# Performance work log

Hardware: AMD Instinct MI355X
Metric: run time of the kernel (lower is better)

The kernel has to match this reference:

```python
import jax, jax.numpy as jnp
import numpy as np

B, S, D, U = 32, 2048, 512, 512

def setup_inputs() -> dict:
    key = jax.random.key(0)
    k1, k2, k3, k4, k5 = jax.random.split(key, 5)
    passage = jax.random.normal(k1, (B, S, D), dtype=jnp.float32)
    hidden = jax.random.normal(k2, (B, D), dtype=jnp.float32)
    mask = jnp.ones((B, S), dtype=jnp.float32)
    # learned params (Dense kernels, glorot-ish scale)
    W1 = jax.random.normal(k3, (D, U), dtype=jnp.float32) / np.sqrt(D)
    W2 = jax.random.normal(k4, (D, U), dtype=jnp.float32) / np.sqrt(D)
    Vw = jax.random.normal(k5, (U, 1), dtype=jnp.float32) / np.sqrt(U)
    Vb = jnp.zeros((1,), dtype=jnp.float32)
    return {"passage": passage, "hidden": hidden, "mask": mask,
            "W1": W1, "W2": W2, "Vw": Vw, "Vb": Vb}

def reference(passage, hidden, mask, W1, W2, Vw, Vb):
    # passage: [B,S,D], hidden: [B,D], mask: [B,S]
    h_proj = jnp.einsum('bd,du->bu', hidden, W2)[:, None, :]        # [B,1,U]
    p_proj = jnp.einsum('bsd,du->bsu', passage, W1)                  # [B,S,U]
    score = jnp.einsum('bsu,uo->bso', jnp.tanh(p_proj + h_proj), Vw) + Vb  # [B,S,1]
    score = score + ((1.0 - mask) * -1e30)[:, :, None]
    attention_weights = jax.nn.softmax(score, axis=1)                # [B,S,1]
    context_vector = jnp.sum(attention_weights * passage, axis=1)    # [B,D]
    return context_vector, attention_weights
```

## Files before the change

kernel.cpp:

```cpp
#include <hip/hip_runtime.h>
#include <hip/hip_bf16.h>
#include <cstddef>


#define NB 32
#define NS 2048
#define ND 512
#define NU 512

typedef __bf16 bf16_t;
typedef __bf16 bf16x8 __attribute__((ext_vector_type(8)));
typedef float floatx4 __attribute__((ext_vector_type(4)));

__device__ __forceinline__ void dma16(const void* g, void* l) {
    __builtin_amdgcn_global_load_lds(
        (const __attribute__((address_space(1))) unsigned int*)g,
        (__attribute__((address_space(3))) unsigned int*)l, 16, 0, 0);
}

__global__ __launch_bounds__(256) void prep_kernel(
    const float* __restrict__ W1, bf16_t* __restrict__ W1p,
    const float* __restrict__ hidden, const float* __restrict__ W2,
    float* __restrict__ hproj) {
    if (blockIdx.x < 128) {
        int wave = threadIdx.x >> 6, lane = threadIdx.x & 63;
        int f = (blockIdx.x << 2) + wave;
        int kc = f >> 5, ng = f & 31;
        int q = lane >> 4, c = lane & 15;
        const float* src = W1 + (kc * 32 + q * 8) * 512 + ng * 16 + c;
        bf16x8 w;
#pragma unroll
        for (int jj = 0; jj < 8; ++jj) w[jj] = (bf16_t)src[jj * 512];
        ((bf16x8*)W1p)[(f << 6) + lane] = w;
    } else {
        __shared__ float h[ND];
        __shared__ float part[256];
        int bi = blockIdx.x - 128;
        int b = bi >> 2, ug = bi & 3;
        int t = threadIdx.x;
        h[t] = hidden[b * ND + t];
        h[t + 256] = hidden[b * ND + t + 256];
        __syncthreads();
        int u = (ug << 7) + (t & 127);
        int d0 = (t >> 7) << 8;
        float acc = 0.f;
#pragma unroll 8
        for (int d = d0; d < d0 + 256; ++d) acc = fmaf(h[d], W2[d * NU + u], acc);
        part[t] = acc;
        __syncthreads();
        if (t < 128) hproj[b * NU + u] = part[t] + part[t + 128];
    }
}

__global__ __launch_bounds__(256, 3) void score_kernel(
    const float* __restrict__ passage, const bf16_t* __restrict__ W1p,
    const float* __restrict__ hproj, const float* __restrict__ Vw,
    const float* __restrict__ Vb, float* __restrict__ scores) {
    __shared__ float ring[4 * 64 * 32];
    __shared__ float red[4 * 64];
    const int tid = threadIdx.x;
    const int wave = tid >> 6, lane = tid & 63;
    const int q = lane >> 4, c = lane & 15;
    const int bid = blockIdx.x;
    const int mblk = ((bid >> 4) << 3) + (bid & 7);
    const int nhalf = (bid >> 3) & 1;
    const int m0 = mblk * 64;
    const int b = m0 >> 11;
    const int ng0 = (nhalf << 4) + (wave << 2);
    const bf16x8* Wq = (const bf16x8*)W1p;

    const int ch0 = wave * 2;
    const int r0 = ch0 * 8 + (lane >> 3);
    const int k0 = ((lane & 7) - r0) & 7;
    const int r1 = r0 + 8;
    const int k1 = ((lane & 7) - r1) & 7;
    const float* g0 = passage + (size_t)(m0 + r0) * ND + k0 * 4;
    const float* g1 = passage + (size_t)(m0 + r1) * ND + k1 * 4;

#define DMA_SLICE(slice) do {                                         \
        char* _l = (char*)ring + ((slice) & 3) * 8192 + ch0 * 1024;   \
        dma16(g0 + (slice) * 32, _l);                                 \
        dma16(g1 + (slice) * 32, _l + 1024);                          \
    } while (0)

    DMA_SLICE(0);
    DMA_SLICE(1);
    DMA_SLICE(2);
    asm volatile("" ::: "memory");
    bf16x8 bb[2][4];
#pragma unroll
    for (int j = 0; j < 4; ++j)
        bb[0][j] = Wq[((ng0 + j) << 6) + lane];
    asm volatile("s_waitcnt vmcnt(8)" ::: "memory");
    __builtin_amdgcn_s_barrier();

    floatx4 acc[4][4];
#pragma unroll
    for (int i = 0; i < 4; ++i)
#pragma unroll
        for (int j = 0; j < 4; ++j) { floatx4 z = {0.f, 0.f, 0.f, 0.f}; acc[i][j] = z; }

#pragma unroll
    for (int kc = 0; kc < 16; ++kc) {
        if (kc < 15) {
#pragma unroll
            for (int j = 0; j < 4; ++j)
                bb[(kc + 1) & 1][j] = Wq[((((kc + 1) << 5) + ng0 + j) << 6) + lane];
        }
        if (kc + 3 < 16) DMA_SLICE(kc + 3);

        const float* sl = ring + (kc & 3) * 2048;
#pragma unroll
        for (int i = 0; i < 4; ++i) {
            int r = i * 16 + c;
            const float* rp = sl + r * 32;
            floatx4 lo = *(const floatx4*)(rp + (((q << 1) + r) & 7) * 4);
            floatx4 hi = *(const floatx4*)(rp + (((q << 1) + 1 + r) & 7) * 4);
            bf16x8 a;
            a[0] = (bf16_t)lo[0]; a[1] = (bf16_t)lo[1];
            a[2] = (bf16_t)lo[2]; a[3] = (bf16_t)lo[3];
            a[4] = (bf16_t)hi[0]; a[5] = (bf16_t)hi[1];
            a[6] = (bf16_t)hi[2]; a[7] = (bf16_t)hi[3];
#pragma unroll
            for (int j = 0; j < 4; ++j)
                acc[i][j] = __builtin_amdgcn_mfma_f32_16x16x32_bf16(a, bb[kc & 1][j], acc[i][j], 0, 0, 0);
        }
        if (kc < 15) {
            asm volatile("s_waitcnt vmcnt(8)" ::: "memory");
            __builtin_amdgcn_s_barrier();
        }
    }
#undef DMA_SLICE

    float sp[4][4];
#pragma unroll
    for (int i = 0; i < 4; ++i)
#pragma unroll
        for (int r = 0; r < 4; ++r) sp[i][r] = 0.f;
#pragma unroll
    for (int j = 0; j < 4; ++j) {
        int n = ((ng0 + j) << 4) + c;
        float hp = hproj[(b << 9) + n];
        float vw = Vw[n];
#pragma unroll
        for (int i = 0; i < 4; ++i)
#pragma unroll
            for (int r = 0; r < 4; ++r) {
                float x = acc[i][j][r] + hp;
                float e = __expf(2.0f * x);
                float t = 1.0f - 2.0f * __builtin_amdgcn_rcpf(e + 1.0f);
                sp[i][r] = fmaf(t, vw, sp[i][r]);
            }
    }
#pragma unroll
    for (int off = 1; off < 16; off <<= 1)
#pragma unroll
        for (int i = 0; i < 4; ++i)
#pragma unroll
            for (int r = 0; r < 4; ++r)
                sp[i][r] += __shfl_xor(sp[i][r], off, 64);

    if (c == 0) {
#pragma unroll
        for (int i = 0; i < 4; ++i)
#pragma unroll
            for (int r = 0; r < 4; ++r)
                red[(wave << 6) + i * 16 + q * 4 + r] = sp[i][r];
    }
    __syncthreads();
    if (tid < 64) {
        float s = red[tid] + red[64 + tid] + red[128 + tid] + red[192 + tid];
        if (nhalf == 0) s += Vb[0];
        atomicAdd(&scores[m0 + tid], s);
    }
}

__global__ __launch_bounds__(1024) void softmax_kernel(
    const float* __restrict__ mask, float* __restrict__ attn) {
    __shared__ float smx[16], ssm[16];
    int b = blockIdx.x, tid = threadIdx.x;
    int wave = tid >> 6, lane = tid & 63;
    const int base = b * NS;
    float v0 = attn[base + tid] + (1.0f - mask[base + tid]) * (-1e30f);
    float v1 = attn[base + 1024 + tid] + (1.0f - mask[base + 1024 + tid]) * (-1e30f);
    float mx = fmaxf(v0, v1);
#pragma unroll
    for (int off = 1; off < 64; off <<= 1) mx = fmaxf(mx, __shfl_xor(mx, off, 64));
    if (lane == 0) smx[wave] = mx;
    __syncthreads();
    mx = smx[0];
#pragma unroll
    for (int w = 1; w < 16; ++w) mx = fmaxf(mx, smx[w]);
    v0 = __expf(v0 - mx); v1 = __expf(v1 - mx);
    float sum = v0 + v1;
#pragma unroll
    for (int off = 1; off < 64; off <<= 1) sum += __shfl_xor(sum, off, 64);
    if (lane == 0) ssm[wave] = sum;
    __syncthreads();
    sum = 0.f;
#pragma unroll
    for (int w = 0; w < 16; ++w) sum += ssm[w];
    float inv = 1.0f / sum;
    attn[base + tid] = v0 * inv;
    attn[base + 1024 + tid] = v1 * inv;
}

__global__ __launch_bounds__(512) void context_kernel(
    const float* __restrict__ passage, const float* __restrict__ attn,
    float* __restrict__ ctx) {
    __shared__ float4 part[512];
    int bb = blockIdx.x >> 5, sc = blockIdx.x & 31, t = threadIdx.x;
    int col = t & 127, qh = t >> 7;
    const float4* p = (const float4*)(passage + (((size_t)bb * NS + sc * 64 + qh * 16) << 9));
    const float* wp = attn + bb * NS + sc * 64 + qh * 16;
    float ax = 0.f, ay = 0.f, az = 0.f, aw = 0.f;
#pragma unroll 16
    for (int s = 0; s < 16; ++s) {
        float w = wp[s];
        float4 v = p[(size_t)s * 128 + col];
        ax = fmaf(w, v.x, ax); ay = fmaf(w, v.y, ay);
        az = fmaf(w, v.z, az); aw = fmaf(w, v.w, aw);
    }
    float4 mine; mine.x = ax; mine.y = ay; mine.z = az; mine.w = aw;
    part[t] = mine;
    __syncthreads();
    if (t < 128) {
        float4 o1 = part[t + 128], o2 = part[t + 256], o3 = part[t + 384];
        float* dst = ctx + bb * ND + t * 4;
        atomicAdd(dst + 0, ax + o1.x + o2.x + o3.x);
        atomicAdd(dst + 1, ay + o1.y + o2.y + o3.y);
        atomicAdd(dst + 2, az + o1.z + o2.z + o3.z);
        atomicAdd(dst + 3, aw + o1.w + o2.w + o3.w);
    }
}

extern "C" void kernel_launch(void* const* d_in, const int* in_sizes, int n_in,
                              void* d_out, int out_size, void* d_ws, size_t ws_size,
                              hipStream_t stream) {
    const float* passage = (const float*)d_in[0];
    const float* hidden  = (const float*)d_in[1];
    const float* mask    = (const float*)d_in[2];
    const float* W1      = (const float*)d_in[3];
    const float* W2      = (const float*)d_in[4];
    const float* Vw      = (const float*)d_in[5];
    const float* Vb      = (const float*)d_in[6];

    float* ctx  = (float*)d_out;
    float* attn = (float*)d_out + NB * ND;

    bf16_t* W1p  = (bf16_t*)d_ws;
    float* hproj = (float*)((char*)d_ws + (size_t)NU * ND * 2);

    hipMemsetAsync(ctx, 0, (size_t)NB * (ND + NS) * sizeof(float), stream);
    prep_kernel<<<dim3(256), dim3(256), 0, stream>>>(W1, W1p, hidden, W2, hproj);
    score_kernel<<<dim3(2 * NB * NS / 64), dim3(256), 0, stream>>>(passage, W1p, hproj, Vw, Vb, attn);
    softmax_kernel<<<dim3(NB), dim3(1024), 0, stream>>>(mask, attn);
    context_kernel<<<dim3(NB * 32), dim3(512), 0, stream>>>(passage, attn, ctx);
}
```

Measured before the change: 270.5 us.

## Preload whole bf16 passage tile into LDS instead of streaming fp32 ring

The score kernel no longer streams fp32 passage slices through a 4-deep async global-to-LDS ring with per-slice barriers. Each block now loads its full 64x512 passage tile up front, converts it to bf16 once, and stores it in a 64 KB XOR-swizzled LDS buffer. The K loop then runs barrier-free on direct bf16 LDS reads. This removes the repeated per-iteration conversion and synchronisation, but gives up load/compute overlap within a block, and the larger LDS footprint lowers occupancy (launch bounds drop to 2 blocks per CU).

```diff
diff --git a/kernel.cpp b/kernel.cpp
--- a/kernel.cpp
+++ b/kernel.cpp
@@ -11,12 +11,6 @@
 typedef __bf16 bf16_t;
 typedef __bf16 bf16x8 __attribute__((ext_vector_type(8)));
 typedef float floatx4 __attribute__((ext_vector_type(4)));
-
-__device__ __forceinline__ void dma16(const void* g, void* l) {
-    __builtin_amdgcn_global_load_lds(
-        (const __attribute__((address_space(1))) unsigned int*)g,
-        (__attribute__((address_space(3))) unsigned int*)l, 16, 0, 0);
-}
 
 __global__ __launch_bounds__(256) void prep_kernel(
     const float* __restrict__ W1, bf16_t* __restrict__ W1p,
@@ -52,11 +46,11 @@
     }
 }
 
-__global__ __launch_bounds__(256, 3) void score_kernel(
+__global__ __launch_bounds__(256, 2) void score_kernel(
     const float* __restrict__ passage, const bf16_t* __restrict__ W1p,
     const float* __restrict__ hproj, const float* __restrict__ Vw,
     const float* __restrict__ Vb, float* __restrict__ scores) {
-    __shared__ float ring[4 * 64 * 32];
+    __shared__ bf16_t As[64 * 512];
     __shared__ float red[4 * 64];
     const int tid = threadIdx.x;
     const int wave = tid >> 6, lane = tid & 63;
@@ -69,30 +63,27 @@
     const int ng0 = (nhalf << 4) + (wave << 2);
     const bf16x8* Wq = (const bf16x8*)W1p;
 
-    const int ch0 = wave * 2;
-    const int r0 = ch0 * 8 + (lane >> 3);
-    const int k0 = ((lane & 7) - r0) & 7;
-    const int r1 = r0 + 8;
-    const int k1 = ((lane & 7) - r1) & 7;
-    const float* g0 = passage + (size_t)(m0 + r0) * ND + k0 * 4;
-    const float* g1 = passage + (size_t)(m0 + r1) * ND + k1 * 4;
-
-#define DMA_SLICE(slice) do {                                         \
-        char* _l = (char*)ring + ((slice) & 3) * 8192 + ch0 * 1024;   \
-        dma16(g0 + (slice) * 32, _l);                                 \
-        dma16(g1 + (slice) * 32, _l + 1024);                          \
-    } while (0)
-
-    DMA_SLICE(0);
-    DMA_SLICE(1);
-    DMA_SLICE(2);
-    asm volatile("" ::: "memory");
+#pragma unroll 4
+    for (int cc = 0; cc < 16; ++cc) {
+        int row = (cc << 2) + wave;
+        const float* g = passage + ((size_t)(m0 + row) << 9) + (lane << 3);
+        floatx4 f0 = *(const floatx4*)g;
+        floatx4 f1 = *(const floatx4*)(g + 4);
+        bf16x8 v;
+        v[0] = (bf16_t)f0[0]; v[1] = (bf16_t)f0[1];
+        v[2] = (bf16_t)f0[2]; v[3] = (bf16_t)f0[3];
+        v[4] = (bf16_t)f1[0]; v[5] = (bf16_t)f1[1];
+        v[6] = (bf16_t)f1[2]; v[7] = (bf16_t)f1[3];
+        unsigned kb = (unsigned)(lane << 4) ^ (unsigned)((row & 7) << 4);
+        *(bf16x8*)((char*)As + row * 1024 + kb) = v;
+    }
+
     bf16x8 bb[2][4];
 #pragma unroll
     for (int j = 0; j < 4; ++j)
         bb[0][j] = Wq[((ng0 + j) << 6) + lane];
-    asm volatile("s_waitcnt vmcnt(8)" ::: "memory");
-    __builtin_amdgcn_s_barrier();
+
+    __syncthreads();
 
     floatx4 acc[4][4];
 #pragma unroll
@@ -107,30 +98,16 @@
             for (int j = 0; j < 4; ++j)
                 bb[(kc + 1) & 1][j] = Wq[((((kc + 1) << 5) + ng0 + j) << 6) + lane];
         }
-        if (kc + 3 < 16) DMA_SLICE(kc + 3);
-
-        const float* sl = ring + (kc & 3) * 2048;
 #pragma unroll
         for (int i = 0; i < 4; ++i) {
-            int r = i * 16 + c;
-            const float* rp = sl + r * 32;
-            floatx4 lo = *(const floatx4*)(rp + (((q << 1) + r) & 7) * 4);
-            floatx4 hi = *(const floatx4*)(rp + (((q << 1) + 1 + r) & 7) * 4);
-            bf16x8 a;
-            a[0] = (bf16_t)lo[0]; a[1] = (bf16_t)lo[1];
-            a[2] = (bf16_t)lo[2]; a[3] = (bf16_t)lo[3];
-            a[4] = (bf16_t)hi[0]; a[5] = (bf16_t)hi[1];
-            a[6] = (bf16_t)hi[2]; a[7] = (bf16_t)hi[3];
+            int row = (i << 4) + c;
+            unsigned kb = (unsigned)((kc << 6) + (q << 4)) ^ (unsigned)((row & 7) << 4);
+            bf16x8 a = *(const bf16x8*)((const char*)As + row * 1024 + kb);
 #pragma unroll
             for (int j = 0; j < 4; ++j)
                 acc[i][j] = __builtin_amdgcn_mfma_f32_16x16x32_bf16(a, bb[kc & 1][j], acc[i][j], 0, 0, 0);
         }
-        if (kc < 15) {
-            asm volatile("s_waitcnt vmcnt(8)" ::: "memory");
-            __builtin_amdgcn_s_barrier();
-        }
-    }
-#undef DMA_SLICE
+    }
 
     float sp[4][4];
 #pragma unroll
@@ -165,7 +142,7 @@
         for (int i = 0; i < 4; ++i)
 #pragma unroll
             for (int r = 0; r < 4; ++r)
-                red[(wave << 6) + i * 16 + q * 4 + r] = sp[i][r];
+                red[(wave << 6) + (i << 4) + (q << 2) + r] = sp[i][r];
     }
     __syncthreads();
     if (tid < 64) {
```

After: 285.1 us. 5.4% more time.
